# Kernel optimization log

Measured on AMD Instinct MI355X. Metric: run time of the kernel, lower is better.

## Reference

```python
import jax, jax.numpy as jnp
import numpy as np

N_NODES = 10000
N_EDGES = 320000
IN_FEATS = 500
CONV_DIMS = [500, 256, 256]
FC_DIMS = [256, 128, 40]
BN_EPS = 1e-5


def setup_inputs() -> dict:
    key = jax.random.key(0)
    ks = jax.random.split(key, 16)
    inp = {
        "x": jax.random.normal(ks[0], (N_NODES, IN_FEATS), dtype=jnp.float32),
        "edge_index": jax.random.randint(ks[1], (2, N_EDGES), 0, N_NODES, dtype=jnp.int64),
    }
    # conv layer params: Linear W [in,out], b [out]; BatchNorm gamma/beta [out]
    ki = 2
    for li in range(len(CONV_DIMS) - 1):
        d_in, d_out = CONV_DIMS[li], CONV_DIMS[li + 1]
        s = 1.0 / np.sqrt(d_in)
        inp[f"conv_W{li}"] = jax.random.uniform(ks[ki], (d_in, d_out), jnp.float32, -s, s); ki += 1
        inp[f"conv_b{li}"] = jax.random.uniform(ks[ki], (d_out,), jnp.float32, -s, s); ki += 1
        inp[f"bn_g{li}"] = jnp.ones((d_out,), jnp.float32)
        inp[f"bn_b{li}"] = jnp.zeros((d_out,), jnp.float32)
    for li in range(len(FC_DIMS) - 1):
        d_in, d_out = FC_DIMS[li], FC_DIMS[li + 1]
        s = 1.0 / np.sqrt(d_in)
        inp[f"fc_W{li}"] = jax.random.uniform(ks[ki], (d_in, d_out), jnp.float32, -s, s); ki += 1
        inp[f"fc_b{li}"] = jax.random.uniform(ks[ki], (d_out,), jnp.float32, -s, s); ki += 1
    return inp


def _degree(edge_index, n, dtype):
    # Faithful to: A = eye(N); A[i,j] = 1 per edge (set semantics dedupes repeats).
    A = jnp.eye(n, dtype=dtype).at[edge_index[0], edge_index[1]].set(1.0)
    return A.sum(axis=1)  # deg_i = rowsum of A


def _batchnorm(h, g, b):
    # training-mode BatchNorm1d: batch stats, biased variance
    mean = h.mean(axis=0)
    var = h.var(axis=0)
    return (h - mean) * jax.lax.rsqrt(var + BN_EPS) * g + b


def reference(x, edge_index, conv_W0, conv_b0, bn_g0, bn_b0,
              conv_W1, conv_b1, bn_g1, bn_b1,
              fc_W0, fc_b0, fc_W1, fc_b1):
    n = x.shape[0]
    deg = _degree(edge_index, n, x.dtype)
    # D = sqrt(diag(deg)) is a diagonal matrix, so elementwise D*A*D = diag(deg);
    # mm(D*A*D, x) == deg[:, None] * x (exactly the original math).
    h = x
    for W, b, g, beta in ((conv_W0, conv_b0, bn_g0, bn_b0),
                          (conv_W1, conv_b1, bn_g1, bn_b1)):
        h = (deg[:, None] * h) @ W + b
        h = jax.nn.relu(h)
        h = _batchnorm(h, g, beta)
        # dropout: identity at inference
    for W, b in ((fc_W0, fc_b0), (fc_W1, fc_b1)):
        h = jax.nn.relu(h @ W + b)  # original appends ReLU after every fc, incl. last
    return h
```

## Files before the change

kernel.cpp:

```cpp
#include <hip/hip_runtime.h>

#define NN 10000
#define NE 320000
#define MP 10112
#define BN_EPS 1e-5f

#define NRANGE 64
#define BROWS 160
#define NBUCK 128
#define HBITS 5120
#define HWORDS 160
#define SUBCAP 128
#define EPB   5000

typedef __attribute__((ext_vector_type(8))) short short8;
typedef __attribute__((ext_vector_type(4))) float f32x4;
typedef unsigned short u16;

__device__ __forceinline__ void split1(float v, u16& h, u16& l) {
    unsigned int u = __float_as_uint(v);
    h = (u16)(u >> 16);
    float hf = __uint_as_float(u & 0xFFFF0000u);
    l = (u16)(__float_as_uint(v - hf) >> 16);
}

__device__ __forceinline__ void gll16(const void* g, void* l) {
    __builtin_amdgcn_global_load_lds(
        (const __attribute__((address_space(1))) unsigned int*)g,
        (__attribute__((address_space(3))) unsigned int*)l, 16, 0, 0);
}

__device__ void splitW_dev(const float* __restrict__ W, int K, int N, int Kp, int Np,
                           u16* __restrict__ Wt, int bx, int by, char* smem) {
    float (*tile)[65] = (float(*)[65])smem;
    int t = threadIdx.x;
    int bk = bx * 64, bn = by * 64;
    #pragma unroll
    for (int p = 0; p < 4; ++p) {
        int kk = (t >> 4) + p * 16;
        int nc = (t & 15) * 4;
        int k = bk + kk;
        float4 v = {0.f, 0.f, 0.f, 0.f};
        if (k < K && bn + nc + 3 < N)
            v = *(const float4*)&W[(size_t)k * N + bn + nc];
        tile[kk][nc] = v.x; tile[kk][nc + 1] = v.y;
        tile[kk][nc + 2] = v.z; tile[kk][nc + 3] = v.w;
    }
    __syncthreads();
    int nn = t >> 2;
    int kk0 = (t & 3) * 16;
    u16 hs[16], ls[16];
    #pragma unroll
    for (int j = 0; j < 16; ++j) split1(tile[kk0 + j][nn], hs[j], ls[j]);
    size_t ob = (size_t)(bn + nn) * Kp + bk + kk0;
    size_t lo = (size_t)Np * Kp;
    *(short8*)&Wt[ob] = *(short8*)hs;
    *(short8*)&Wt[ob + 8] = *(short8*)&hs[8];
    *(short8*)&Wt[lo + ob] = *(short8*)ls;
    *(short8*)&Wt[lo + ob + 8] = *(short8*)&ls[8];
}

__global__ __launch_bounds__(256)
void scatter_prep(const int* __restrict__ ei,
                  unsigned* __restrict__ bucketArr, unsigned* __restrict__ cnts,
                  float* __restrict__ stats,
                  const float* __restrict__ W0, const float* __restrict__ fW1,
                  u16* __restrict__ W0t, u16* __restrict__ fW1t) {
    __shared__ char smem[16704];
    __shared__ unsigned cnt[NBUCK];
    int b = blockIdx.x;
    int t = threadIdx.x;
    if (b < 64) {
        if (t < NBUCK) cnt[t] = 0;
        __syncthreads();
        int base = b * EPB;
        #pragma unroll
        for (int k = 0; k < 20; ++k) {
            int el = t + k * 256;
            if (el < EPB) {
                int e = base + el;
                unsigned i = (unsigned)ei[e], j = (unsigned)ei[NE + e];
                unsigned bk = (i / BROWS) * 2 + (j >= HBITS ? 1u : 0u);
                unsigned key = (i << 14) | j;
                unsigned pos = atomicAdd(&cnt[bk], 1u);
                if (pos < SUBCAP)
                    bucketArr[((size_t)bk << 13) + ((unsigned)b << 7) + pos] = key;
            }
        }
        __syncthreads();
        if (t < NBUCK) cnts[(t << 6) + b] = min(cnt[t], (unsigned)SUBCAP);
    } else if (b < 96) {
        int idx = b - 64;
        splitW_dev(W0, 500, 256, 512, 256, W0t, idx & 7, idx >> 3, smem);
    } else {
        int base = (b - 96) * 512;
        stats[base + t] = 0.f;
        stats[base + 256 + t] = 0.f;
        splitW_dev(fW1, 128, 40, 128, 64, fW1t, b - 96, 0, smem);
    }
}

__global__ __launch_bounds__(256)
void bucket_degree(const unsigned* __restrict__ bucketArr,
                   const unsigned* __restrict__ cnts,
                   float* __restrict__ degh) {
    __shared__ unsigned lbm[BROWS * HWORDS];
    int b = blockIdx.x, t = threadIdx.x;
    int rr = b >> 1, h = b & 1;
    int row0 = rr * BROWS;
    {
        uint4* z = (uint4*)lbm;
        #pragma unroll
        for (int i = 0; i < 25; ++i) z[t + i * 256] = (uint4){0u, 0u, 0u, 0u};
    }
    __syncthreads();
    for (int r = t; r < BROWS; r += 256) {
        int i = row0 + r;
        if (i < NN && ((i >= HBITS) == (h == 1))) {
            int jj = i - h * HBITS;
            atomicOr(&lbm[r * HWORDS + (jj >> 5)], 1u << (jj & 31));
        }
    }
    {
        int sb = t >> 2, kl = t & 3;
        unsigned n = cnts[(b << 6) + sb];
        const unsigned* keys = bucketArr + ((size_t)b << 13) + ((unsigned)sb << 7);
        for (unsigned k = kl; k < n; k += 4) {
            unsigned key = keys[k];
            unsigned i = key >> 14, j = key & 0x3FFFu;
            unsigned r = i - row0;
            unsigned jj = j - h * HBITS;
            atomicOr(&lbm[r * HWORDS + (jj >> 5)], 1u << (jj & 31));
        }
    }
    __syncthreads();
    #pragma unroll
    for (int pass = 0; pass < 3; ++pass) {
        int r = pass * 64 + (t >> 2), wl = t & 3;
        if (r >= BROWS) break;
        int i = row0 + r;
        int c = 0;
        const uint4* rp = (const uint4*)&lbm[r * HWORDS + wl * 40];
        #pragma unroll
        for (int m = 0; m < 10; ++m) {
            uint4 v = rp[m];
            c += __popc(v.x) + __popc(v.y) + __popc(v.z) + __popc(v.w);
        }
        c += __shfl_down(c, 1, 4);
        c += __shfl_down(c, 2, 4);
        if (wl == 0 && i < MP) degh[h * MP + i] = (float)c;
    }
}

__global__ __launch_bounds__(256, 4)
void conv0_gemm(const float* __restrict__ x,
                const u16* __restrict__ Bhi, const u16* __restrict__ Blo,
                const float* __restrict__ degh, const float* __restrict__ bias,
                float* __restrict__ stats,
                u16* __restrict__ Ohi, u16* __restrict__ Olo) {
    __shared__ char smem[32768];
    __shared__ float sdeg[64];
    const int Kp = 512, M = NN, No = 256;
    const int b = blockIdx.x;
    const int xcd = b & 7, g = b >> 3;
    const int bx = g & 3, by = (g >> 2) * 8 + xcd;
    if (by >= 158) return;
    const int t = threadIdx.x;
    const int lane = t & 63;
    const int w = t >> 6;
    const int q = lane >> 4;
    const int l16 = lane & 15;
    const int m7 = l16 & 7;
    const int row0 = by * 64;
    const int col0 = bx * 64;

    const u16* srcs[4];
    unsigned dstoff[4];
    #pragma unroll
    for (int i = 0; i < 4; ++i) {
        int j = w + (i & 1) * 4;
        int plane = i >> 1;
        int r = j * 8 + (lane >> 3);
        int c = (lane & 7) ^ (r & 7);
        srcs[i] = (plane ? Blo : Bhi) + (size_t)(col0 + r) * Kp + c * 8;
        dstoff[i] = 16384 + plane * 8192 + j * 1024;
    }
    #pragma unroll
    for (int i = 0; i < 4; ++i) { gll16(srcs[i], smem + dstoff[i]); srcs[i] += 64; }

    const int rn = t & 63;
    const int c4 = t >> 6;
    const int ch0 = c4 * 2;
    float vals[16];
    {
        int row = row0 + rn;
        const float* xp = x + (size_t)row * 500 + c4 * 16;
        #pragma unroll
        for (int m = 0; m < 4; ++m) {
            float4 v = {0.f, 0.f, 0.f, 0.f};
            if (row < NN && (c4 * 16 + m * 4) < 500)
                v = *(const float4*)(xp + m * 4);
            vals[m * 4 + 0] = v.x; vals[m * 4 + 1] = v.y;
            vals[m * 4 + 2] = v.z; vals[m * 4 + 3] = v.w;
        }
    }

    if (t < 64) sdeg[t] = degh[row0 + t] + degh[MP + row0 + t];

    f32x4 acc[4];
    #pragma unroll
    for (int s = 0; s < 4; ++s) acc[s] = (f32x4){0.f, 0.f, 0.f, 0.f};

    for (int k0 = 0; k0 < Kp; k0 += 64) {
        {
            u16 hs[16], ls[16];
            #pragma unroll
            for (int i2 = 0; i2 < 16; ++i2) split1(vals[i2], hs[i2], ls[i2]);
            unsigned o0 = rn * 128 + ((ch0 ^ (rn & 7)) * 16);
            unsigned o1 = rn * 128 + (((ch0 + 1) ^ (rn & 7)) * 16);
            *(short8*)(smem + o0) = *(short8*)&hs[0];
            *(short8*)(smem + o1) = *(short8*)&hs[8];
            *(short8*)(smem + 8192 + o0) = *(short8*)&ls[0];
            *(short8*)(smem + 8192 + o1) = *(short8*)&ls[8];
        }
        __syncthreads();
        short8 ah[2], al[2], bh[2][4], bl[2][4];
        #pragma unroll
        for (int kc = 0; kc < 2; ++kc) {
            int aoff = (w * 16 + l16) * 128 + (((kc * 4 + q) ^ m7) * 16);
            ah[kc] = *(const short8*)(smem + aoff);
            al[kc] = *(const short8*)(smem + 8192 + aoff);
            #pragma unroll
            for (int s = 0; s < 4; ++s) {
                int boff = (s * 16 + l16) * 128 + (((kc * 4 + q) ^ m7) * 16);
                bh[kc][s] = *(const short8*)(smem + 16384 + boff);
                bl[kc][s] = *(const short8*)(smem + 24576 + boff);
            }
        }
        __syncthreads();
        if (k0 + 64 < Kp) {
            #pragma unroll
            for (int i = 0; i < 4; ++i) { gll16(srcs[i], smem + dstoff[i]); srcs[i] += 64; }
            int row = row0 + rn;
            const float* xp = x + (size_t)row * 500 + k0 + 64 + c4 * 16;
            #pragma unroll
            for (int m = 0; m < 4; ++m) {
                float4 v = {0.f, 0.f, 0.f, 0.f};
                if (row < NN && (k0 + 64 + c4 * 16 + m * 4) < 500)
                    v = *(const float4*)(xp + m * 4);
                vals[m * 4 + 0] = v.x; vals[m * 4 + 1] = v.y;
                vals[m * 4 + 2] = v.z; vals[m * 4 + 3] = v.w;
            }
        }
        #pragma unroll
        for (int kc = 0; kc < 2; ++kc)
            #pragma unroll
            for (int s = 0; s < 4; ++s) {
                acc[s] = __builtin_amdgcn_mfma_f32_16x16x32_bf16(al[kc], bh[kc][s], acc[s], 0, 0, 0);
                acc[s] = __builtin_amdgcn_mfma_f32_16x16x32_bf16(ah[kc], bl[kc][s], acc[s], 0, 0, 0);
                acc[s] = __builtin_amdgcn_mfma_f32_16x16x32_bf16(ah[kc], bh[kc][s], acc[s], 0, 0, 0);
            }
    }

    int growb = row0 + w * 16 + q * 4;
    float dgv[4];
    #pragma unroll
    for (int r = 0; r < 4; ++r) {
        int grow = growb + r;
        dgv[r] = (grow < M) ? sdeg[grow - row0] : 0.f;
    }
    #pragma unroll
    for (int s = 0; s < 4; ++s) {
        int gc = col0 + s * 16 + l16;
        float bia = bias[gc];
        float s_sum = 0.f, ss_sum = 0.f;
        #pragma unroll
        for (int r = 0; r < 4; ++r) {
            int grow = growb + r;
            bool real = grow < M;
            float v = fmaxf(fmaf(dgv[r], acc[s][r], bia), 0.f);
            if (!real) v = 0.f;
            s_sum += v; ss_sum += v * v;
            float vo = v * dgv[r];
            u16 h, l; split1(vo, h, l);
            Ohi[(size_t)grow * No + gc] = h;
            Olo[(size_t)grow * No + gc] = l;
        }
        s_sum  += __shfl_xor(s_sum, 16);  s_sum  += __shfl_xor(s_sum, 32);
        ss_sum += __shfl_xor(ss_sum, 16); ss_sum += __shfl_xor(ss_sum, 32);
        if (lane < 16) {
            atomicAdd(&stats[gc], s_sum);
            atomicAdd(&stats[256 + gc], ss_sum);
        }
    }
}

__global__ __launch_bounds__(256, 4)
void conv1_fold(const u16* __restrict__ Ahi, const u16* __restrict__ Alo,
                const float* __restrict__ W1, const float* __restrict__ stats0,
                const float* __restrict__ g0, const float* __restrict__ bb0,
                const float* __restrict__ b1, const float* __restrict__ degh,
                float* __restrict__ stats1, u16* __restrict__ Ohi, u16* __restrict__ Olo) {
    __shared__ char smem[32768];
    __shared__ float scl[256], sh[256], cred[256], cvec[64];
    const int Kp = 256, M = NN, No = 256;
    const int b = blockIdx.x;
    const int xcd = b & 7, g = b >> 3;
    const int bx = g & 3, by = (g >> 2) * 8 + xcd;
    if (by >= 158) return;
    const int t = threadIdx.x;
    const int lane = t & 63;
    const int w = t >> 6;
    const int q = lane >> 4;
    const int l16 = lane & 15;
    const int m7 = l16 & 7;
    const int row0 = by * 64;
    const int col0 = bx * 64;

    const u16* srcs[4];
    unsigned dstoff[4];
    #pragma unroll
    for (int i = 0; i < 4; ++i) {
        int gi = w + i * 4;
        int plane = gi >> 3, j = gi & 7;
        int r = j * 8 + (lane >> 3);
        int c = (lane & 7) ^ (r & 7);
        srcs[i] = (plane ? Alo : Ahi) + (size_t)(row0 + r) * Kp + c * 8;
        dstoff[i] = plane * 8192 + j * 1024;
    }
    #pragma unroll
    for (int i = 0; i < 4; ++i) { gll16(srcs[i], smem + dstoff[i]); srcs[i] += 64; }

    {
        float mean = stats0[t] * (1.f / NN);
        float var = stats0[256 + t] * (1.f / NN) - mean * mean;
        float s = g0[t] * rsqrtf(var + BN_EPS);
        scl[t] = s;
        sh[t] = bb0[t] - mean * s;
    }
    __syncthreads();
    {
        float s = 0.f;
        int n = col0 + (t & 63);
        #pragma unroll 8
        for (int k = (t >> 6); k < 256; k += 4)
            s += sh[k] * W1[(size_t)k * 256 + n];
        cred[t] = s;
        __syncthreads();
        if (t < 64) cvec[t] = cred[t] + cred[t + 64] + cred[t + 128] + cred[t + 192];
    }
    const int bn = t & 63;
    const int kb = (t >> 6) * 16;
    const int ch0 = (t >> 6) * 2;
    float vals[16];
    {
        const float* wp = W1 + (size_t)kb * 256 + col0 + bn;
        #pragma unroll
        for (int i = 0; i < 16; ++i) vals[i] = wp[(size_t)i * 256] * scl[kb + i];
    }

    f32x4 acc[4];
    #pragma unroll
    for (int s = 0; s < 4; ++s) acc[s] = (f32x4){0.f, 0.f, 0.f, 0.f};

    for (int k0 = 0; k0 < Kp; k0 += 64) {
        {
            u16 hs[16], ls[16];
            #pragma unroll
            for (int i = 0; i < 16; ++i) split1(vals[i], hs[i], ls[i]);
            unsigned o0 = bn * 128 + ((ch0 ^ (bn & 7)) * 16);
            unsigned o1 = bn * 128 + (((ch0 + 1) ^ (bn & 7)) * 16);
            *(short8*)(smem + 16384 + o0) = *(short8*)&hs[0];
            *(short8*)(smem + 16384 + o1) = *(short8*)&hs[8];
            *(short8*)(smem + 24576 + o0) = *(short8*)&ls[0];
            *(short8*)(smem + 24576 + o1) = *(short8*)&ls[8];
        }
        __syncthreads();
        short8 ah[2], al[2], bh[2][4], bl[2][4];
        #pragma unroll
        for (int kc = 0; kc < 2; ++kc) {
            int aoff = (w * 16 + l16) * 128 + (((kc * 4 + q) ^ m7) * 16);
            ah[kc] = *(const short8*)(smem + aoff);
            al[kc] = *(const short8*)(smem + 8192 + aoff);
            #pragma unroll
            for (int s = 0; s < 4; ++s) {
                int boff = (s * 16 + l16) * 128 + (((kc * 4 + q) ^ m7) * 16);
                bh[kc][s] = *(const short8*)(smem + 16384 + boff);
                bl[kc][s] = *(const short8*)(smem + 24576 + boff);
            }
        }
        __syncthreads();
        if (k0 + 64 < Kp) {
            #pragma unroll
            for (int i = 0; i < 4; ++i) { gll16(srcs[i], smem + dstoff[i]); srcs[i] += 64; }
            const float* wp = W1 + (size_t)(k0 + 64 + kb) * 256 + col0 + bn;
            #pragma unroll
            for (int i = 0; i < 16; ++i) vals[i] = wp[(size_t)i * 256] * scl[k0 + 64 + kb + i];
        }
        #pragma unroll
        for (int kc = 0; kc < 2; ++kc)
            #pragma unroll
            for (int s = 0; s < 4; ++s) {
                acc[s] = __builtin_amdgcn_mfma_f32_16x16x32_bf16(al[kc], bh[kc][s], acc[s], 0, 0, 0);
                acc[s] = __builtin_amdgcn_mfma_f32_16x16x32_bf16(ah[kc], bl[kc][s], acc[s], 0, 0, 0);
                acc[s] = __builtin_amdgcn_mfma_f32_16x16x32_bf16(ah[kc], bh[kc][s], acc[s], 0, 0, 0);
            }
    }

    int growb = row0 + w * 16 + q * 4;
    float dgv[4];
    #pragma unroll
    for (int r = 0; r < 4; ++r) {
        int grow = growb + r;
        dgv[r] = (grow < M) ? (degh[grow] + degh[MP + grow]) : 0.f;
    }
    #pragma unroll
    for (int s = 0; s < 4; ++s) {
        int gc = col0 + s * 16 + l16;
        float bia = b1[gc];
        float cv = cvec[s * 16 + l16];
        float s_sum = 0.f, ss_sum = 0.f;
        #pragma unroll
        for (int r = 0; r < 4; ++r) {
            int grow = growb + r;
            bool real = grow < M;
            float v = fmaxf(fmaf(dgv[r], cv, acc[s][r] + bia), 0.f);
            if (!real) v = 0.f;
            s_sum += v; ss_sum += v * v;
            u16 h, l; split1(v, h, l);
            Ohi[(size_t)grow * No + gc] = h;
            Olo[(size_t)grow * No + gc] = l;
        }
        s_sum  += __shfl_xor(s_sum, 16);  s_sum  += __shfl_xor(s_sum, 32);
        ss_sum += __shfl_xor(ss_sum, 16); ss_sum += __shfl_xor(ss_sum, 32);
        if (lane < 16) {
            atomicAdd(&stats1[gc], s_sum);
            atomicAdd(&stats1[256 + gc], ss_sum);
        }
    }
}

__global__ __launch_bounds__(256, 4)
void fc0_fold(const u16* __restrict__ Ahi, const u16* __restrict__ Alo,
              const float* __restrict__ fW0, const float* __restrict__ stats1,
              const float* __restrict__ g1, const float* __restrict__ bb1,
              const float* __restrict__ fb0,
              u16* __restrict__ Ohi, u16* __restrict__ Olo) {
    __shared__ char smem[32768];
    __shared__ float scl[256], sh[256], cred[256], biasf[64];
    const int Kp = 256, M = NN, No = 128;
    const int b = blockIdx.x;
    const int xcd = b & 7, g = b >> 3;
    const int bx = g & 1, by = (g >> 1) * 8 + xcd;
    if (by >= 158) return;
    const int t = threadIdx.x;
    const int lane = t & 63;
    const int w = t >> 6;
    const int q = lane >> 4;
    const int l16 = lane & 15;
    const int m7 = l16 & 7;
    const int row0 = by * 64;
    const int col0 = bx * 64;

    const u16* srcs[4];
    unsigned dstoff[4];
    #pragma unroll
    for (int i = 0; i < 4; ++i) {
        int gi = w + i * 4;
        int plane = gi >> 3, j = gi & 7;
        int r = j * 8 + (lane >> 3);
        int c = (lane & 7) ^ (r & 7);
        srcs[i] = (plane ? Alo : Ahi) + (size_t)(row0 + r) * Kp + c * 8;
        dstoff[i] = plane * 8192 + j * 1024;
    }
    #pragma unroll
    for (int i = 0; i < 4; ++i) { gll16(srcs[i], smem + dstoff[i]); srcs[i] += 64; }

    {
        float mean = stats1[t] * (1.f / NN);
        float var = stats1[256 + t] * (1.f / NN) - mean * mean;
        float s = g1[t] * rsqrtf(var + BN_EPS);
        scl[t] = s;
        sh[t] = bb1[t] - mean * s;
    }
    __syncthreads();
    {
        float s = 0.f;
        int n = col0 + (t & 63);
        #pragma unroll 8
        for (int k = (t >> 6); k < 256; k += 4)
            s += sh[k] * fW0[(size_t)k * 128 + n];
        cred[t] = s;
        __syncthreads();
        if (t < 64)
            biasf[t] = fb0[col0 + t] + cred[t] + cred[t + 64] + cred[t + 128] + cred[t + 192];
    }
    const int bn = t & 63;
    const int kb = (t >> 6) * 16;
    const int ch0 = (t >> 6) * 2;
    float vals[16];
    {
        const float* wp = fW0 + (size_t)kb * 128 + col0 + bn;
        #pragma unroll
        for (int i = 0; i < 16; ++i) vals[i] = wp[(size_t)i * 128] * scl[kb + i];
    }

    f32x4 acc[4];
    #pragma unroll
    for (int s = 0; s < 4; ++s) acc[s] = (f32x4){0.f, 0.f, 0.f, 0.f};

    for (int k0 = 0; k0 < Kp; k0 += 64) {
        {
            u16 hs[16], ls[16];
            #pragma unroll
            for (int i = 0; i < 16; ++i) split1(vals[i], hs[i], ls[i]);
            unsigned o0 = bn * 128 + ((ch0 ^ (bn & 7)) * 16);
            unsigned o1 = bn * 128 + (((ch0 + 1) ^ (bn & 7)) * 16);
            *(short8*)(smem + 16384 + o0) = *(short8*)&hs[0];
            *(short8*)(smem + 16384 + o1) = *(short8*)&hs[8];
            *(short8*)(smem + 24576 + o0) = *(short8*)&ls[0];
            *(short8*)(smem + 24576 + o1) = *(short8*)&ls[8];
        }
        __syncthreads();
        short8 ah[2], al[2], bh[2][4], bl[2][4];
        #pragma unroll
        for (int kc = 0; kc < 2; ++kc) {
            int aoff = (w * 16 + l16) * 128 + (((kc * 4 + q) ^ m7) * 16);
            ah[kc] = *(const short8*)(smem + aoff);
            al[kc] = *(const short8*)(smem + 8192 + aoff);
            #pragma unroll
            for (int s = 0; s < 4; ++s) {
                int boff = (s * 16 + l16) * 128 + (((kc * 4 + q) ^ m7) * 16);
                bh[kc][s] = *(const short8*)(smem + 16384 + boff);
                bl[kc][s] = *(const short8*)(smem + 24576 + boff);
            }
        }
        __syncthreads();
        if (k0 + 64 < Kp) {
            #pragma unroll
            for (int i = 0; i < 4; ++i) { gll16(srcs[i], smem + dstoff[i]); srcs[i] += 64; }
            const float* wp = fW0 + (size_t)(k0 + 64 + kb) * 128 + col0 + bn;
            #pragma unroll
            for (int i = 0; i < 16; ++i) vals[i] = wp[(size_t)i * 128] * scl[k0 + 64 + kb + i];
        }
        #pragma unroll
        for (int kc = 0; kc < 2; ++kc)
            #pragma unroll
            for (int s = 0; s < 4; ++s) {
                acc[s] = __builtin_amdgcn_mfma_f32_16x16x32_bf16(al[kc], bh[kc][s], acc[s], 0, 0, 0);
                acc[s] = __builtin_amdgcn_mfma_f32_16x16x32_bf16(ah[kc], bl[kc][s], acc[s], 0, 0, 0);
                acc[s] = __builtin_amdgcn_mfma_f32_16x16x32_bf16(ah[kc], bh[kc][s], acc[s], 0, 0, 0);
            }
    }

    int growb = row0 + w * 16 + q * 4;
    #pragma unroll
    for (int s = 0; s < 4; ++s) {
        int gc = col0 + s * 16 + l16;
        float bia = biasf[s * 16 + l16];
        #pragma unroll
        for (int r = 0; r < 4; ++r) {
            int grow = growb + r;
            float v = fmaxf(acc[s][r] + bia, 0.f);
            if (grow >= M) v = 0.f;
            u16 h, l; split1(v, h, l);
            Ohi[(size_t)grow * No + gc] = h;
            Olo[(size_t)grow * No + gc] = l;
        }
    }
}

__global__ __launch_bounds__(256, 3)
void fc1_gemm(const u16* __restrict__ Ahi, const u16* __restrict__ Alo,
              const u16* __restrict__ Bhi, const u16* __restrict__ Blo,
              const float* __restrict__ bias, float* __restrict__ out) {
    __shared__ char smem[32768];
    const int Kp = 128, M = NN, N = 40, No = 40;
    const int t = threadIdx.x;
    const int lane = t & 63;
    const int w = t >> 6;
    const int q = lane >> 4;
    const int l16 = lane & 15;
    const int m7 = l16 & 7;
    const int row0 = blockIdx.x * 64;
    const int col0 = 0;

    const u16* bases[4] = {Ahi, Alo, Bhi, Blo};
    const u16* srcs[8];
    unsigned dstoff[8];
    #pragma unroll
    for (int i = 0; i < 8; ++i) {
        int gi = w + i * 4;
        int reg = i >> 1;
        int j = gi & 7;
        int rb = (reg < 2) ? row0 : col0;
        int r = j * 8 + (lane >> 3);
        int c = (lane & 7) ^ (r & 7);
        srcs[i] = bases[reg] + (size_t)(rb + r) * Kp + c * 8;
        dstoff[i] = reg * 8192 + j * 1024;
    }

    f32x4 acc[4];
    #pragma unroll
    for (int s = 0; s < 4; ++s) acc[s] = (f32x4){0.f, 0.f, 0.f, 0.f};

    #pragma unroll
    for (int i = 0; i < 8; ++i) { gll16(srcs[i], smem + dstoff[i]); srcs[i] += 64; }

    for (int k0 = 0; k0 < Kp; k0 += 64) {
        __syncthreads();
        short8 ah[2], al[2], bh[2][4], bl[2][4];
        #pragma unroll
        for (int kc = 0; kc < 2; ++kc) {
            int aoff = (w * 16 + l16) * 128 + (((kc * 4 + q) ^ m7) * 16);
            ah[kc] = *(const short8*)(smem + aoff);
            al[kc] = *(const short8*)(smem + 8192 + aoff);
            #pragma unroll
            for (int s = 0; s < 4; ++s) {
                int boff = (s * 16 + l16) * 128 + (((kc * 4 + q) ^ m7) * 16);
                bh[kc][s] = *(const short8*)(smem + 16384 + boff);
                bl[kc][s] = *(const short8*)(smem + 24576 + boff);
            }
        }
        __syncthreads();
        if (k0 + 64 < Kp) {
            #pragma unroll
            for (int i = 0; i < 8; ++i) { gll16(srcs[i], smem + dstoff[i]); srcs[i] += 64; }
        }
        #pragma unroll
        for (int kc = 0; kc < 2; ++kc)
            #pragma unroll
            for (int s = 0; s < 4; ++s) {
                acc[s] = __builtin_amdgcn_mfma_f32_16x16x32_bf16(al[kc], bh[kc][s], acc[s], 0, 0, 0);
                acc[s] = __builtin_amdgcn_mfma_f32_16x16x32_bf16(ah[kc], bl[kc][s], acc[s], 0, 0, 0);
                acc[s] = __builtin_amdgcn_mfma_f32_16x16x32_bf16(ah[kc], bh[kc][s], acc[s], 0, 0, 0);
            }
    }

    int growb = row0 + w * 16 + q * 4;
    #pragma unroll
    for (int s = 0; s < 4; ++s) {
        int gc = col0 + s * 16 + l16;
        if (gc >= N) continue;
        float bia = bias[gc];
        #pragma unroll
        for (int r = 0; r < 4; ++r) {
            int grow = growb + r;
            if (grow < M)
                out[(size_t)grow * No + gc] = fmaxf(acc[s][r] + bia, 0.f);
        }
    }
}


extern "C" void kernel_launch(void* const* d_in, const int* in_sizes, int n_in,
                              void* d_out, int out_size, void* d_ws, size_t ws_size,
                              hipStream_t stream) {
    const float* x   = (const float*)d_in[0];
    const int*   ei  = (const int*)d_in[1];
    const float* W0  = (const float*)d_in[2];
    const float* b0  = (const float*)d_in[3];
    const float* g0  = (const float*)d_in[4];
    const float* bb0 = (const float*)d_in[5];
    const float* W1  = (const float*)d_in[6];
    const float* b1  = (const float*)d_in[7];
    const float* g1  = (const float*)d_in[8];
    const float* bb1 = (const float*)d_in[9];
    const float* fW0 = (const float*)d_in[10];
    const float* fb0 = (const float*)d_in[11];
    const float* fW1 = (const float*)d_in[12];
    const float* fb1 = (const float*)d_in[13];
    float* out = (float*)d_out;

    char* ws = (char*)d_ws;
    auto carve = [&](size_t bytes) { char* q = ws; ws += (bytes + 255) & ~(size_t)255; return q; };

    float* stats = (float*)carve(4096);
    unsigned* cnts = (unsigned*)carve((size_t)NBUCK * 64 * 4);
    float* degh = (float*)carve((size_t)2 * MP * 4);
    unsigned* bucketArr = (unsigned*)carve((size_t)NBUCK * 64 * SUBCAP * 4);
    u16* W0t    = (u16*)carve((size_t)2 * 256 * 512 * 2);
    u16* fW1t   = (u16*)carve((size_t)2 * 64 * 128 * 2);
    u16* H1     = (u16*)carve((size_t)2 * MP * 256 * 2);
    u16* H2     = (u16*)carve((size_t)2 * MP * 256 * 2);
    u16* H3     = (u16*)carve((size_t)2 * MP * 128 * 2);

    dim3 blk(256);

    scatter_prep<<<98, blk, 0, stream>>>(ei, bucketArr, cnts, stats, W0, fW1, W0t, fW1t);
    bucket_degree<<<NBUCK, blk, 0, stream>>>(bucketArr, cnts, degh);
    conv0_gemm<<<640, blk, 0, stream>>>(
        x, W0t, W0t + 256 * 512, degh, b0, stats, H1, H1 + (size_t)MP * 256);
    conv1_fold<<<640, blk, 0, stream>>>(
        H1, H1 + (size_t)MP * 256, W1, stats, g0, bb0, b1, degh,
        stats + 512, H2, H2 + (size_t)MP * 256);
    fc0_fold<<<320, blk, 0, stream>>>(
        H2, H2 + (size_t)MP * 256, fW0, stats + 512, g1, bb1, fb0,
        H3, H3 + (size_t)MP * 128);
    fc1_gemm<<<158, blk, 0, stream>>>(
        H3, H3 + (size_t)MP * 128, fW1t, fW1t + 64 * 128, fb1, out);
}
```

Measured before the change: 188.4 us.

## Stream conv0 x tiles into LDS via async global-to-LDS loads with prefetch

Replaces the per-thread register loads of the fp32 x tile in conv0_gemm with async global-to-LDS 16-byte loads into a new swizzled 16 KB LDS region, issued two k-steps ahead. Out-of-range rows and columns point at a zeroed pad buffer set up in scatter_prep. The aim is to hide x load latency behind the MFMA loop. The cost is more LDS per block (48 KB) and a launch bound lowered from 4 to 3 waves per SIMD, which may reduce occupancy.

Result: faster. 177.7 us (-5.7%).

```diff
diff --git a/kernel.cpp b/kernel.cpp
--- a/kernel.cpp
+++ b/kernel.cpp
@@ -63,7 +63,7 @@
 __global__ __launch_bounds__(256)
 void scatter_prep(const int* __restrict__ ei,
                   unsigned* __restrict__ bucketArr, unsigned* __restrict__ cnts,
-                  float* __restrict__ stats,
+                  float* __restrict__ stats, float* __restrict__ zpad,
                   const float* __restrict__ W0, const float* __restrict__ fW1,
                   u16* __restrict__ W0t, u16* __restrict__ fW1t) {
     __shared__ char smem[16704];
@@ -96,6 +96,7 @@
         int base = (b - 96) * 512;
         stats[base + t] = 0.f;
         stats[base + 256 + t] = 0.f;
+        if (b == 96 && t < 64) zpad[t] = 0.f;
         splitW_dev(fW1, 128, 40, 128, 64, fW1t, b - 96, 0, smem);
     }
 }
@@ -152,13 +153,13 @@
     }
 }
 
-__global__ __launch_bounds__(256, 4)
-void conv0_gemm(const float* __restrict__ x,
+__global__ __launch_bounds__(256, 3)
+void conv0_gemm(const float* __restrict__ x, const float* __restrict__ zpad,
                 const u16* __restrict__ Bhi, const u16* __restrict__ Blo,
                 const float* __restrict__ degh, const float* __restrict__ bias,
                 float* __restrict__ stats,
                 u16* __restrict__ Ohi, u16* __restrict__ Olo) {
-    __shared__ char smem[32768];
+    __shared__ char smem[49152];
     __shared__ float sdeg[64];
     const int Kp = 512, M = NN, No = 256;
     const int b = blockIdx.x;
@@ -185,27 +186,57 @@
         srcs[i] = (plane ? Blo : Bhi) + (size_t)(col0 + r) * Kp + c * 8;
         dstoff[i] = 16384 + plane * 8192 + j * 1024;
     }
-    #pragma unroll
-    for (int i = 0; i < 4; ++i) { gll16(srcs[i], smem + dstoff[i]); srcs[i] += 64; }
+
+    int xrow[4];
+    int xcol[4];
+    unsigned xdst[4];
+    #pragma unroll
+    for (int i = 0; i < 4; ++i) {
+        int slab = w * 4 + i;
+        int row = slab * 4 + (lane >> 4);
+        int cl = (lane & 15) ^ (row & 15);
+        xrow[i] = row0 + row;
+        xcol[i] = cl * 4;
+        xdst[i] = 32768 + slab * 1024;
+    }
+
+    #pragma unroll
+    for (int i = 0; i < 4; ++i) gll16(srcs[i], smem + dstoff[i]);
+    #pragma unroll
+    for (int i = 0; i < 4; ++i) {
+        int col = xcol[i];
+        const float* s = (xrow[i] < NN && col < 500)
+                       ? x + (size_t)xrow[i] * 500 + col : zpad;
+        gll16(s, smem + xdst[i]);
+    }
+
+    if (t < 64) sdeg[t] = degh[row0 + t] + degh[MP + row0 + t];
+
+    __syncthreads();
 
     const int rn = t & 63;
     const int c4 = t >> 6;
     const int ch0 = c4 * 2;
     float vals[16];
-    {
-        int row = row0 + rn;
-        const float* xp = x + (size_t)row * 500 + c4 * 16;
-        #pragma unroll
-        for (int m = 0; m < 4; ++m) {
-            float4 v = {0.f, 0.f, 0.f, 0.f};
-            if (row < NN && (c4 * 16 + m * 4) < 500)
-                v = *(const float4*)(xp + m * 4);
-            vals[m * 4 + 0] = v.x; vals[m * 4 + 1] = v.y;
-            vals[m * 4 + 2] = v.z; vals[m * 4 + 3] = v.w;
-        }
-    }
-
-    if (t < 64) sdeg[t] = degh[row0 + t] + degh[MP + row0 + t];
+    #pragma unroll
+    for (int m = 0; m < 4; ++m) {
+        int phys = (c4 * 4 + m) ^ (rn & 15);
+        float4 v = *(const float4*)(smem + 32768 + rn * 256 + phys * 16);
+        vals[m * 4 + 0] = v.x; vals[m * 4 + 1] = v.y;
+        vals[m * 4 + 2] = v.z; vals[m * 4 + 3] = v.w;
+    }
+
+    __syncthreads();
+
+    #pragma unroll
+    for (int i = 0; i < 4; ++i) {
+        int col = 64 + xcol[i];
+        const float* s = (xrow[i] < NN && col < 500)
+                       ? x + (size_t)xrow[i] * 500 + col : zpad;
+        gll16(s, smem + xdst[i]);
+    }
+    #pragma unroll
+    for (int i = 0; i < 4; ++i) srcs[i] += 64;
 
     f32x4 acc[4];
     #pragma unroll
@@ -232,24 +263,33 @@
             al[kc] = *(const short8*)(smem + 8192 + aoff);
             #pragma unroll
             for (int s = 0; s < 4; ++s) {
-                int boff = (s * 16 + l16) * 128 + (((kc * 4 + q) ^ m7) * 16);
-                bh[kc][s] = *(const short8*)(smem + 16384 + boff);
-                bl[kc][s] = *(const short8*)(smem + 24576 + boff);
-            }
-        }
-        __syncthreads();
-        if (k0 + 64 < Kp) {
-            #pragma unroll
-            for (int i = 0; i < 4; ++i) { gll16(srcs[i], smem + dstoff[i]); srcs[i] += 64; }
-            int row = row0 + rn;
-            const float* xp = x + (size_t)row * 500 + k0 + 64 + c4 * 16;
+                int boff = 16384 + (s * 16 + l16) * 128 + (((kc * 4 + q) ^ m7) * 16);
+                bh[kc][s] = *(const short8*)(smem + boff);
+                bl[kc][s] = *(const short8*)(smem + 8192 + boff);
+            }
+        }
+        bool more = (k0 + 64 < Kp);
+        if (more) {
             #pragma unroll
             for (int m = 0; m < 4; ++m) {
-                float4 v = {0.f, 0.f, 0.f, 0.f};
-                if (row < NN && (k0 + 64 + c4 * 16 + m * 4) < 500)
-                    v = *(const float4*)(xp + m * 4);
+                int phys = (c4 * 4 + m) ^ (rn & 15);
+                float4 v = *(const float4*)(smem + 32768 + rn * 256 + phys * 16);
                 vals[m * 4 + 0] = v.x; vals[m * 4 + 1] = v.y;
                 vals[m * 4 + 2] = v.z; vals[m * 4 + 3] = v.w;
+            }
+        }
+        __syncthreads();
+        if (more) {
+            #pragma unroll
+            for (int i = 0; i < 4; ++i) { gll16(srcs[i], smem + dstoff[i]); srcs[i] += 64; }
+            if (k0 + 128 < Kp) {
+                #pragma unroll
+                for (int i = 0; i < 4; ++i) {
+                    int col = k0 + 128 + xcol[i];
+                    const float* s = (xrow[i] < NN && col < 500)
+                                   ? x + (size_t)xrow[i] * 500 + col : zpad;
+                    gll16(s, smem + xdst[i]);
+                }
             }
         }
         #pragma unroll
@@ -676,6 +716,7 @@
     auto carve = [&](size_t bytes) { char* q = ws; ws += (bytes + 255) & ~(size_t)255; return q; };
 
     float* stats = (float*)carve(4096);
+    float* zpad  = (float*)carve(1024);
     unsigned* cnts = (unsigned*)carve((size_t)NBUCK * 64 * 4);
     float* degh = (float*)carve((size_t)2 * MP * 4);
     unsigned* bucketArr = (unsigned*)carve((size_t)NBUCK * 64 * SUBCAP * 4);
@@ -687,10 +728,10 @@
 
     dim3 blk(256);
 
-    scatter_prep<<<98, blk, 0, stream>>>(ei, bucketArr, cnts, stats, W0, fW1, W0t, fW1t);
+    scatter_prep<<<98, blk, 0, stream>>>(ei, bucketArr, cnts, stats, zpad, W0, fW1, W0t, fW1t);
     bucket_degree<<<NBUCK, blk, 0, stream>>>(bucketArr, cnts, degh);
     conv0_gemm<<<640, blk, 0, stream>>>(
-        x, W0t, W0t + 256 * 512, degh, b0, stats, H1, H1 + (size_t)MP * 256);
+        x, zpad, W0t, W0t + 256 * 512, degh, b0, stats, H1, H1 + (size_t)MP * 256);
     conv1_fold<<<640, blk, 0, stream>>>(
         H1, H1 + (size_t)MP * 256, W1, stats, g0, bb0, b1, degh,
         stats + 512, H2, H2 + (size_t)MP * 256);
```
